# Performance work log

Hardware: AMD Instinct MI355X
Metric: run time of the kernel (lower is better)

## Reference

```python
import jax, jax.numpy as jnp
import numpy as np

L, V, Tctx, D, H, DFF = 4, 32000, 1024, 1024, 16, 4096
HD = D // H
B, T = 2, 1024


def _ln(x, w, b):
    mu = jnp.mean(x, axis=-1, keepdims=True)
    var = jnp.var(x, axis=-1, keepdims=True)
    return (x - mu) * jax.lax.rsqrt(var + 1e-5) * w + b


def setup_inputs() -> dict:
    key = jax.random.key(0)
    ks = jax.random.split(key, 8)
    s = 0.02
    return {
        "idx": jax.random.randint(ks[0], (B, T), 0, V),
        "wte": jax.random.normal(ks[1], (V, D), jnp.float32) * s,
        "wpe": jax.random.normal(ks[2], (Tctx, D), jnp.float32) * s,
        "ln1_w": jnp.ones((L, D), jnp.float32),
        "ln1_b": jnp.zeros((L, D), jnp.float32),
        "qkv_w": jax.random.normal(ks[3], (L, 3 * D, D), jnp.float32) * s,
        "qkv_b": jnp.zeros((L, 3 * D), jnp.float32),
        "proj_w": jax.random.normal(ks[4], (L, D, D), jnp.float32) * s,
        "proj_b": jnp.zeros((L, D), jnp.float32),
        "ln2_w": jnp.ones((L, D), jnp.float32),
        "ln2_b": jnp.zeros((L, D), jnp.float32),
        "fc1_w": jax.random.normal(ks[5], (L, DFF, D), jnp.float32) * s,
        "fc1_b": jnp.zeros((L, DFF), jnp.float32),
        "fc2_w": jax.random.normal(ks[6], (L, D, DFF), jnp.float32) * s,
        "fc2_b": jnp.zeros((L, D), jnp.float32),
        "lnf_w": jnp.ones((D,), jnp.float32),
        "lnf_b": jnp.zeros((D,), jnp.float32),
    }


def reference(idx, wte, wpe, ln1_w, ln1_b, qkv_w, qkv_b, proj_w, proj_b,
              ln2_w, ln2_b, fc1_w, fc1_b, fc2_w, fc2_b, lnf_w, lnf_b):
    b, t = idx.shape
    x = wte[idx] + wpe[:t]  # (B,T,D); dropout=0 (eval)
    scale = 1.0 / jnp.sqrt(jnp.float32(HD))
    causal = jnp.tril(jnp.ones((t, t), bool))  # (T,T)

    def block(x, p):
        (l1w, l1b, qw, qb, pw, pb, l2w, l2b, f1w, f1b, f2w, f2b) = p
        h = _ln(x, l1w, l1b)
        qkv = h @ qw.T + qb  # (B,T,3D)
        q, k, v = jnp.split(qkv, 3, axis=-1)
        q = q.reshape(b, t, H, HD)
        k = k.reshape(b, t, H, HD)
        v = v.reshape(b, t, H, HD)
        att = jnp.einsum('bqhd,bkhd->bhqk', q, k) * scale
        att = jnp.where(causal, att, -jnp.inf)
        att = jax.nn.softmax(att, axis=-1)
        y = jnp.einsum('bhqk,bkhd->bqhd', att, v).reshape(b, t, D)
        x = x + y @ pw.T + pb
        h2 = _ln(x, l2w, l2b)
        h2 = jax.nn.gelu(h2 @ f1w.T + f1b, approximate=False)
        x = x + h2 @ f2w.T + f2b
        return x, None

    params = (ln1_w, ln1_b, qkv_w, qkv_b, proj_w, proj_b,
              ln2_w, ln2_b, fc1_w, fc1_b, fc2_w, fc2_b)
    x, _ = jax.lax.scan(block, x, params)
    x = _ln(x, lnf_w, lnf_b)
    logits = x @ wte.T  # weight-tied lm_head
    return logits
```

## Files before the change

### kernel.cpp

```cpp
#include <hip/hip_runtime.h>
#include <hip/hip_bf16.h>
#include <cstdint>
#include <cstddef>

using hb = __hip_bfloat16;
typedef __bf16 bf16x8 __attribute__((ext_vector_type(8)));
typedef float f32x4 __attribute__((ext_vector_type(4)));
typedef const __attribute__((address_space(1))) void* gptr_t;
typedef __attribute__((address_space(3))) void* lptr_t;

namespace {
constexpr int L_ = 4, V_ = 32000, D_ = 1024, H_ = 16, DFF_ = 4096, HD_ = 64;
constexpr int B_ = 2, T_ = 1024;
constexpr int BT = B_ * T_;
constexpr int PSTR = 56;
constexpr int MTILES = BT / 128;
}

__device__ __forceinline__ void cast_range(const float* __restrict__ in,
                                           hb* __restrict__ out, int n4,
                                           int base, int stride) {
  for (int i = base; i < n4; i += stride) {
    float4 v = reinterpret_cast<const float4*>(in)[i];
    union { hb h[4]; ushort4 u; } t;
    t.h[0] = __float2bfloat16(v.x);
    t.h[1] = __float2bfloat16(v.y);
    t.h[2] = __float2bfloat16(v.z);
    t.h[3] = __float2bfloat16(v.w);
    reinterpret_cast<ushort4*>(out)[i] = t.u;
  }
}

__global__ __launch_bounds__(256) void k_cast5(
    const float* s0, hb* d0, int n0, const float* s1, hb* d1, int n1,
    const float* s2, hb* d2, int n2, const float* s3, hb* d3, int n3,
    const float* s4, hb* d4, int n4) {
  const int base = blockIdx.x * 256 + threadIdx.x;
  const int stride = gridDim.x * 256;
  cast_range(s0, d0, n0, base, stride);
  cast_range(s1, d1, n1, base, stride);
  cast_range(s2, d2, n2, base, stride);
  cast_range(s3, d3, n3, base, stride);
  cast_range(s4, d4, n4, base, stride);
}

__global__ __launch_bounds__(256) void k_embed_ln(const int* __restrict__ idx,
                                                  const float* __restrict__ wte,
                                                  const float* __restrict__ wpe,
                                                  const float* __restrict__ w,
                                                  const float* __restrict__ b,
                                                  float* __restrict__ x,
                                                  hb* __restrict__ out) {
  const int row = blockIdx.x;
  const int tid = threadIdx.x;
  const int t = row & (T_ - 1);
  const int tok = idx[row];
  const float4 a = reinterpret_cast<const float4*>(wte + (size_t)tok * D_)[tid];
  const float4 p = reinterpret_cast<const float4*>(wpe + (size_t)t * D_)[tid];
  const float4 v = {a.x + p.x, a.y + p.y, a.z + p.z, a.w + p.w};
  reinterpret_cast<float4*>(x + (size_t)row * D_)[tid] = v;
  float s = v.x + v.y + v.z + v.w;
  float ss = v.x * v.x + v.y * v.y + v.z * v.z + v.w * v.w;
#pragma unroll
  for (int o = 32; o; o >>= 1) { s += __shfl_xor(s, o); ss += __shfl_xor(ss, o); }
  __shared__ float rs[4], rss[4];
  const int wid = tid >> 6;
  if ((tid & 63) == 0) { rs[wid] = s; rss[wid] = ss; }
  __syncthreads();
  s = rs[0] + rs[1] + rs[2] + rs[3];
  ss = rss[0] + rss[1] + rss[2] + rss[3];
  const float mu = s * (1.f / D_);
  const float var = ss * (1.f / D_) - mu * mu;
  const float rstd = rsqrtf(var + 1e-5f);
  const float4 wv = reinterpret_cast<const float4*>(w)[tid];
  const float4 bv = reinterpret_cast<const float4*>(b)[tid];
  union { hb h[4]; ushort4 u; } o2;
  o2.h[0] = __float2bfloat16((v.x - mu) * rstd * wv.x + bv.x);
  o2.h[1] = __float2bfloat16((v.y - mu) * rstd * wv.y + bv.y);
  o2.h[2] = __float2bfloat16((v.z - mu) * rstd * wv.z + bv.z);
  o2.h[3] = __float2bfloat16((v.w - mu) * rstd * wv.w + bv.w);
  reinterpret_cast<ushort4*>(out + (size_t)row * D_)[tid] = o2.u;
}

__global__ __launch_bounds__(256) void k_ln(const float* __restrict__ x,
                                            const float* __restrict__ w,
                                            const float* __restrict__ b,
                                            hb* __restrict__ out) {
  const int row = blockIdx.x;
  const int tid = threadIdx.x;
  const float4 v = reinterpret_cast<const float4*>(x + (size_t)row * D_)[tid];
  float s = v.x + v.y + v.z + v.w;
  float ss = v.x * v.x + v.y * v.y + v.z * v.z + v.w * v.w;
#pragma unroll
  for (int o = 32; o; o >>= 1) { s += __shfl_xor(s, o); ss += __shfl_xor(ss, o); }
  __shared__ float rs[4], rss[4];
  const int wid = tid >> 6;
  if ((tid & 63) == 0) { rs[wid] = s; rss[wid] = ss; }
  __syncthreads();
  s = rs[0] + rs[1] + rs[2] + rs[3];
  ss = rss[0] + rss[1] + rss[2] + rss[3];
  const float mu = s * (1.f / D_);
  const float var = ss * (1.f / D_) - mu * mu;
  const float rstd = rsqrtf(var + 1e-5f);
  const float4 wv = reinterpret_cast<const float4*>(w)[tid];
  const float4 bv = reinterpret_cast<const float4*>(b)[tid];
  union { hb h[4]; ushort4 u; } t;
  t.h[0] = __float2bfloat16((v.x - mu) * rstd * wv.x + bv.x);
  t.h[1] = __float2bfloat16((v.y - mu) * rstd * wv.y + bv.y);
  t.h[2] = __float2bfloat16((v.z - mu) * rstd * wv.z + bv.z);
  t.h[3] = __float2bfloat16((v.w - mu) * rstd * wv.w + bv.w);
  reinterpret_cast<ushort4*>(out + (size_t)row * D_)[tid] = t.u;
}

__global__ __launch_bounds__(256) void k_attn(const hb* __restrict__ qkv,
                                              const hb* __restrict__ vt,
                                              hb* __restrict__ y) {
  const int lane = threadIdx.x & 63;
  const int wid = threadIdx.x >> 6;
  const int gw = blockIdx.x * 4 + wid;
  const int qt = 63 - (gw & 63);
  const int bh = gw >> 6;
  const int h = bh & (H_ - 1), b = bh >> 4;
  const int q0 = qt * 16;
  const int lr = lane & 15, g = lane >> 4;

  __shared__ __align__(16) hb plds[4][16 * PSTR];
  hb* pw = plds[wid];

  const size_t qrow = ((size_t)(b * T_ + q0 + lr) * 3 * D_) + (size_t)h * HD_;
  const bf16x8 qa0 = *reinterpret_cast<const bf16x8*>(qkv + qrow + g * 8);
  const bf16x8 qa1 = *reinterpret_cast<const bf16x8*>(qkv + qrow + 32 + g * 8);

  const f32x4 z = {0.f, 0.f, 0.f, 0.f};
  float m[4] = {-1e30f, -1e30f, -1e30f, -1e30f};
  float lsum[4] = {0.f, 0.f, 0.f, 0.f};
  f32x4 o[4];
#pragma unroll
  for (int i = 0; i < 4; ++i) o[i] = z;

  const int nkv = (q0 + 47) >> 5;
  for (int kt = 0; kt < nkv; ++kt) {
    const int kv0 = kt * 32;
    f32x4 s[2];
#pragma unroll
    for (int nt = 0; nt < 2; ++nt) {
      const size_t krow =
          ((size_t)(b * T_ + kv0 + nt * 16 + lr) * 3 * D_) + D_ + (size_t)h * HD_;
      const bf16x8 kb0 = *reinterpret_cast<const bf16x8*>(qkv + krow + g * 8);
      const bf16x8 kb1 = *reinterpret_cast<const bf16x8*>(qkv + krow + 32 + g * 8);
      f32x4 acc = z;
      acc = __builtin_amdgcn_mfma_f32_16x16x32_bf16(qa0, kb0, acc, 0, 0, 0);
      acc = __builtin_amdgcn_mfma_f32_16x16x32_bf16(qa1, kb1, acc, 0, 0, 0);
      s[nt] = acc;
    }
#pragma unroll
    for (int r = 0; r < 4; ++r) {
      const int qg = q0 + g * 4 + r;
      const float s0 = (kv0 + lr <= qg) ? s[0][r] * 0.125f : -1e30f;
      const float s1 = (kv0 + 16 + lr <= qg) ? s[1][r] * 0.125f : -1e30f;
      float rmax = fmaxf(s0, s1);
#pragma unroll
      for (int off = 1; off < 16; off <<= 1) rmax = fmaxf(rmax, __shfl_xor(rmax, off));
      const float mn = fmaxf(m[r], rmax);
      const float c = __expf(m[r] - mn);
      m[r] = mn;
      const float p0 = __expf(s0 - mn);
      const float p1 = __expf(s1 - mn);
      float ps = p0 + p1;
#pragma unroll
      for (int off = 1; off < 16; off <<= 1) ps += __shfl_xor(ps, off);
      lsum[r] = lsum[r] * c + ps;
#pragma unroll
      for (int dt = 0; dt < 4; ++dt) o[dt][r] *= c;
      pw[(g * 4 + r) * PSTR + lr] = __float2bfloat16(p0);
      pw[(g * 4 + r) * PSTR + 16 + lr] = __float2bfloat16(p1);
    }
    const bf16x8 pa = *reinterpret_cast<const bf16x8*>(&pw[lr * PSTR + g * 8]);
#pragma unroll
    for (int dt = 0; dt < 4; ++dt) {
      const bf16x8 vb = *reinterpret_cast<const bf16x8*>(
          vt + ((size_t)bh * HD_ + dt * 16 + lr) * T_ + kv0 + g * 8);
      o[dt] = __builtin_amdgcn_mfma_f32_16x16x32_bf16(pa, vb, o[dt], 0, 0, 0);
    }
  }
#pragma unroll
  for (int dt = 0; dt < 4; ++dt) {
#pragma unroll
    for (int r = 0; r < 4; ++r) {
      const size_t oo =
          ((size_t)(b * T_ + q0 + g * 4 + r) * D_) + h * HD_ + dt * 16 + lr;
      y[oo] = __float2bfloat16(o[dt][r] / lsum[r]);
    }
  }
}

template <int EPI, bool OBF, int BN, bool WVT>
__global__ __launch_bounds__(256) void gemm_bt(const hb* __restrict__ A,
                                               const hb* __restrict__ Bw,
                                               const float* __restrict__ bias,
                                               const float* resid,
                                               void* outv, hb* __restrict__ vt,
                                               int M, int N, int K) {
  constexpr int WMR = (BN == 128) ? 4 : 2;
  __shared__ __align__(16) hb As[2][128 * 32];
  __shared__ __align__(16) hb Bs[2][BN * 32];
  const int tid = threadIdx.x, lane = tid & 63, wid = tid >> 6;

  const int nwg = gridDim.x;
  const int d = blockIdx.x;
  const int wg = (d & 7) * (nwg >> 3) + (d >> 3);
  const int m0 = (wg & (MTILES - 1)) * 128;
  const int n0 = (wg / MTILES) * BN;

  const int wr = (BN == 128) ? (wid >> 1) : wid;
  const int wc = (BN == 128) ? (wid & 1) : 0;

  f32x4 acc[WMR][4];
  const f32x4 z = {0.f, 0.f, 0.f, 0.f};
#pragma unroll
  for (int i = 0; i < WMR; ++i)
#pragma unroll
    for (int j = 0; j < 4; ++j) acc[i][j] = z;

  const int e0 = tid * 8;
  auto stage = [&](int buf, int k0) {
#pragma unroll
    for (int r = 0; r < 2; ++r) {
      const int e = e0 + r * 2048;
      const int row = e >> 5, col = e & 31;
      __builtin_amdgcn_global_load_lds(
          (gptr_t)(A + (size_t)(m0 + row) * K + k0 + col), (lptr_t)(&As[buf][e]), 16, 0, 0);
    }
#pragma unroll
    for (int r = 0; r < BN / 64; ++r) {
      const int e = e0 + r * 2048;
      const int row = e >> 5, col = e & 31;
      __builtin_amdgcn_global_load_lds(
          (gptr_t)(Bw + (size_t)(n0 + row) * K + k0 + col), (lptr_t)(&Bs[buf][e]), 16, 0, 0);
    }
  };

  stage(0, 0);
  stage(1, 32);

  const int nt = K >> 5;
  const int lr = lane & 15, lk = (lane >> 4) * 8;
  for (int t = 0; t < nt; ++t) {
    const int cur = t & 1;
    if (t + 1 < nt) {
      if constexpr (BN == 128)
        asm volatile("s_waitcnt vmcnt(4)" ::: "memory");
      else
        asm volatile("s_waitcnt vmcnt(3)" ::: "memory");
    } else {
      asm volatile("s_waitcnt vmcnt(0)" ::: "memory");
    }
    asm volatile("s_barrier" ::: "memory");

    bf16x8 af[WMR], bfr[4];
#pragma unroll
    for (int i = 0; i < WMR; ++i)
      af[i] = *reinterpret_cast<const bf16x8*>(
          &As[cur][(wr * (WMR * 16) + i * 16 + lr) * 32 + lk]);
#pragma unroll
    for (int j = 0; j < 4; ++j)
      bfr[j] = *reinterpret_cast<const bf16x8*>(
          &Bs[cur][(wc * 64 + j * 16 + lr) * 32 + lk]);
#pragma unroll
    for (int i = 0; i < WMR; ++i)
#pragma unroll
      for (int j = 0; j < 4; ++j)
        acc[i][j] = __builtin_amdgcn_mfma_f32_16x16x32_bf16(af[i], bfr[j], acc[i][j], 0, 0, 0);

    asm volatile("s_waitcnt lgkmcnt(0)" ::: "memory");
    asm volatile("s_barrier" ::: "memory");
    if (t + 2 < nt) stage(cur, (t + 2) * 32);
  }

  const int lc = lane & 15, lr4 = (lane >> 4) * 4;
#pragma unroll
  for (int i = 0; i < WMR; ++i) {
    const int grow0 = m0 + wr * (WMR * 16) + i * 16 + lr4;
#pragma unroll
    for (int j = 0; j < 4; ++j) {
      const int gcol = n0 + wc * 64 + j * 16 + lc;
      const float bv = bias ? bias[gcol] : 0.f;
      union { hb h[4]; ushort4 u; } vv;
#pragma unroll
      for (int r = 0; r < 4; ++r) {
        const size_t oo = (size_t)(grow0 + r) * N + gcol;
        float val = acc[i][j][r] + bv;
        if constexpr (EPI == 1) val += resid[oo];
        if constexpr (EPI == 2) val = 0.5f * val * (1.f + erff(val * 0.70710678118f));
        if constexpr (OBF) {
          const hb hv = __float2bfloat16(val);
          reinterpret_cast<hb*>(outv)[oo] = hv;
          if constexpr (WVT) vv.h[r] = hv;
        } else {
          reinterpret_cast<float*>(outv)[oo] = val;
        }
      }
      if constexpr (WVT) {
        if (gcol >= 2 * D_) {
          const int vcol = gcol - 2 * D_;
          const int b = grow0 >> 10;
          const int t0 = grow0 & (T_ - 1);
          *reinterpret_cast<ushort4*>(
              vt + ((size_t)(b * H_ + (vcol >> 6)) * HD_ + (vcol & 63)) * T_ + t0) =
              vv.u;
        }
      }
    }
  }
}

#define MM16(ABASE, AF, BF)                                                     \
  _Pragma("unroll") for (int i_ = 0; i_ < 4; ++i_)                              \
      _Pragma("unroll") for (int j_ = 0; j_ < 4; ++j_)                          \
          acc[(ABASE) + i_][j_] = __builtin_amdgcn_mfma_f32_16x16x32_bf16(      \
              (AF)[i_], (BF)[j_], acc[(ABASE) + i_][j_], 0, 0, 0);

__global__ __launch_bounds__(512, 2) void gemm_lmhead(const hb* __restrict__ A,
                                                      const hb* __restrict__ Bw,
                                                      float* __restrict__ out) {
  constexpr int K = 1024, N = 32000, NT = K / 32;
  __shared__ __align__(16) hb As[4][256][32];
  __shared__ __align__(16) hb Bs[4][256][32];
  const int tid = threadIdx.x, lane = tid & 63, wid = tid >> 6;
  const int nwg = gridDim.x;
  const int dd = blockIdx.x;
  const int wg = (dd & 7) * (nwg >> 3) + (dd >> 3);
  const int m0 = (wg & 7) * 256;
  const int n0 = (wg >> 3) * 256;
  const int wr = wid >> 2, wc = wid & 3;
  const int lr = lane & 15;
  const int rc8 = (((lane >> 4) ^ ((lr >> 1) & 3)) & 3) * 8;

  f32x4 acc[8][4];
  const f32x4 z = {0.f, 0.f, 0.f, 0.f};
#pragma unroll
  for (int i = 0; i < 8; ++i)
#pragma unroll
    for (int j = 0; j < 4; ++j) acc[i][j] = z;

  const int rr = tid >> 2;
  const int cs = tid & 3;
  const int cc = cs ^ ((tid >> 3) & 3);

  auto stageA = [&](int b, int t) {
#pragma unroll
    for (int q = 0; q < 2; ++q) {
      const int row = q * 128 + rr;
      __builtin_amdgcn_global_load_lds(
          (gptr_t)(A + (size_t)(m0 + row) * K + t * 32 + cc * 8),
          (lptr_t)(&As[b][row][cs * 8]), 16, 0, 0);
    }
  };
  auto stageB = [&](int b, int t) {
#pragma unroll
    for (int q = 0; q < 2; ++q) {
      const int row = q * 128 + rr;
      __builtin_amdgcn_global_load_lds(
          (gptr_t)(Bw + (size_t)(n0 + row) * K + t * 32 + cc * 8),
          (lptr_t)(&Bs[b][row][cs * 8]), 16, 0, 0);
    }
  };
  auto dsA = [&](int b, int mh, bf16x8* af) {
#pragma unroll
    for (int i = 0; i < 4; ++i)
      af[i] = *reinterpret_cast<const bf16x8*>(
          &As[b][wr * 128 + mh * 64 + i * 16 + lr][rc8]);
  };
  auto dsB = [&](int b, bf16x8* bf) {
#pragma unroll
    for (int j = 0; j < 4; ++j)
      bf[j] = *reinterpret_cast<const bf16x8*>(&Bs[b][wc * 64 + j * 16 + lr][rc8]);
  };

  auto tile = [&](int t, bool stg, int vm) {
    const int c = t & 3;
    const int b3 = (t + 3) & 3;
    bf16x8 af[4], bf[4];
    dsA(c, 0, af);
    dsB(c, bf);
    if (stg) stageA(b3, t + 3);
    __builtin_amdgcn_s_barrier();
    asm volatile("s_waitcnt lgkmcnt(0)" ::: "memory");
    __builtin_amdgcn_s_setprio(1);
    MM16(0, af, bf)
    __builtin_amdgcn_s_setprio(0);
    __builtin_amdgcn_s_barrier();
    dsA(c, 1, af);
    if (stg) stageB(b3, t + 3);
    if (vm == 8)
      asm volatile("s_waitcnt vmcnt(8)" ::: "memory");
    else if (vm == 4)
      asm volatile("s_waitcnt vmcnt(4)" ::: "memory");
    else if (vm == 0)
      asm volatile("s_waitcnt vmcnt(0)" ::: "memory");
    __builtin_amdgcn_s_barrier();
    asm volatile("s_waitcnt lgkmcnt(0)" ::: "memory");
    __builtin_amdgcn_s_setprio(1);
    MM16(4, af, bf)
    __builtin_amdgcn_s_setprio(0);
    __builtin_amdgcn_s_barrier();
  };

  stageA(0, 0); stageB(0, 0);
  stageA(1, 1); stageB(1, 1);
  stageA(2, 2); stageB(2, 2);
  asm volatile("s_waitcnt vmcnt(8)" ::: "memory");
  __builtin_amdgcn_s_barrier();

  for (int t = 0; t < NT - 3; ++t) tile(t, true, 8);
  tile(NT - 3, false, 4);
  tile(NT - 2, false, 0);
  tile(NT - 1, false, -1);

  const int lc = lane & 15, lr4 = (lane >> 4) * 4;
#pragma unroll
  for (int i2 = 0; i2 < 8; ++i2) {
    const int grow0 = m0 + wr * 128 + i2 * 16 + lr4;
#pragma unroll
    for (int j = 0; j < 4; ++j) {
      const int gcol = n0 + wc * 64 + j * 16 + lc;
#pragma unroll
      for (int r = 0; r < 4; ++r)
        out[(size_t)(grow0 + r) * N + gcol] = acc[i2][j][r];
    }
  }
}

extern "C" void kernel_launch(void* const* d_in, const int* in_sizes, int n_in,
                              void* d_out, int out_size, void* d_ws, size_t ws_size,
                              hipStream_t stream) {
  const int* idx = (const int*)d_in[0];
  const float* wte = (const float*)d_in[1];
  const float* wpe = (const float*)d_in[2];
  const float* ln1_w = (const float*)d_in[3];
  const float* ln1_b = (const float*)d_in[4];
  const float* qkv_w = (const float*)d_in[5];
  const float* qkv_b = (const float*)d_in[6];
  const float* proj_w = (const float*)d_in[7];
  const float* proj_b = (const float*)d_in[8];
  const float* ln2_w = (const float*)d_in[9];
  const float* ln2_b = (const float*)d_in[10];
  const float* fc1_w = (const float*)d_in[11];
  const float* fc1_b = (const float*)d_in[12];
  const float* fc2_w = (const float*)d_in[13];
  const float* fc2_b = (const float*)d_in[14];
  const float* lnf_w = (const float*)d_in[15];
  const float* lnf_b = (const float*)d_in[16];

  char* ws = (char*)d_ws;
  size_t off = 0;
  auto alloc = [&](size_t bytes) -> void* {
    void* p = ws + off;
    off += (bytes + 255) & ~(size_t)255;
    return p;
  };
  hb* wte_bf = (hb*)alloc((size_t)V_ * D_ * 2);
  hb* qkvw_bf = (hb*)alloc((size_t)L_ * 3 * D_ * D_ * 2);
  hb* projw_bf = (hb*)alloc((size_t)L_ * D_ * D_ * 2);
  hb* fc1w_bf = (hb*)alloc((size_t)L_ * DFF_ * D_ * 2);
  hb* fc2w_bf = (hb*)alloc((size_t)L_ * D_ * DFF_ * 2);
  float* x = (float*)alloc((size_t)BT * D_ * 4);
  hb* hbuf = (hb*)alloc((size_t)BT * D_ * 2);
  hb* qkvbuf = (hb*)alloc((size_t)BT * 3 * D_ * 2);
  hb* ybuf = (hb*)alloc((size_t)BT * D_ * 2);
  hb* gbuf = (hb*)alloc((size_t)BT * DFF_ * 2);
  hb* vtbuf = (hb*)alloc((size_t)B_ * H_ * HD_ * T_ * 2);

  k_cast5<<<4096, 256, 0, stream>>>(
      wte, wte_bf, (int)((size_t)V_ * D_ / 4),
      qkv_w, qkvw_bf, (int)((size_t)L_ * 3 * D_ * D_ / 4),
      proj_w, projw_bf, (int)((size_t)L_ * D_ * D_ / 4),
      fc1_w, fc1w_bf, (int)((size_t)L_ * DFF_ * D_ / 4),
      fc2_w, fc2w_bf, (int)((size_t)L_ * D_ * DFF_ / 4));

  k_embed_ln<<<BT, 256, 0, stream>>>(idx, wte, wpe, ln1_w, ln1_b, x, hbuf);

  for (int l = 0; l < L_; ++l) {
    if (l) k_ln<<<BT, 256, 0, stream>>>(x, ln1_w + l * D_, ln1_b + l * D_, hbuf);
    gemm_bt<0, true, 128, true><<<MTILES * (3 * D_ / 128), 256, 0, stream>>>(
        hbuf, qkvw_bf + (size_t)l * 3 * D_ * D_, qkv_b + (size_t)l * 3 * D_, nullptr,
        qkvbuf, vtbuf, BT, 3 * D_, D_);
    k_attn<<<(B_ * H_ * (T_ / 16)) / 4, 256, 0, stream>>>(qkvbuf, vtbuf, ybuf);
    gemm_bt<1, false, 64, false><<<MTILES * (D_ / 64), 256, 0, stream>>>(
        ybuf, projw_bf + (size_t)l * D_ * D_, proj_b + (size_t)l * D_, x, x, nullptr,
        BT, D_, D_);
    k_ln<<<BT, 256, 0, stream>>>(x, ln2_w + l * D_, ln2_b + l * D_, hbuf);
    gemm_bt<2, true, 128, false><<<MTILES * (DFF_ / 128), 256, 0, stream>>>(
        hbuf, fc1w_bf + (size_t)l * DFF_ * D_, fc1_b + (size_t)l * DFF_, nullptr,
        gbuf, nullptr, BT, DFF_, D_);
    gemm_bt<1, false, 64, false><<<MTILES * (D_ / 64), 256, 0, stream>>>(
        gbuf, fc2w_bf + (size_t)l * D_ * DFF_, fc2_b + (size_t)l * D_, x, x, nullptr,
        BT, D_, DFF_);
  }

  k_ln<<<BT, 256, 0, stream>>>(x, lnf_w, lnf_b, hbuf);
  gemm_lmhead<<<8 * (V_ / 256), 512, 0, stream>>>(hbuf, wte_bf, (float*)d_out);
}
```

Before: 1.268 ms.

## Move V transpose to separate kernel and simplify lm_head to double-buffered pipeline

The V transpose is no longer scattered from the QKV GEMM epilogue. It is done by a new LDS-tiled transpose kernel launched before attention, which adds one launch per layer but makes the V^T writes coalesced. Separately, the lm_head GEMM drops its 4-stage LDS ring with split MFMA phases in favour of 2-stage double buffering, halving LDS use and raising the occupancy hint to 4 blocks per CU. The trade is a shallower prefetch depth, with fewer barriers, in exchange for more resident waves.

```diff
diff --git a/kernel.cpp b/kernel.cpp
--- a/kernel.cpp
+++ b/kernel.cpp
@@ -112,6 +112,27 @@
   reinterpret_cast<ushort4*>(out + (size_t)row * D_)[tid] = t.u;
 }
 
+__global__ __launch_bounds__(256) void k_vtrans(const hb* __restrict__ qkv,
+                                                hb* __restrict__ vt) {
+  __shared__ __align__(16) hb tile[64][66];
+  const int bh = blockIdx.x;
+  const int b = bh >> 4, h = bh & (H_ - 1);
+  const int t0 = blockIdx.y * 64;
+  const int tid = threadIdx.x;
+  const int tl = tid >> 2, dc = (tid & 3) * 16;
+  const hb* src = qkv + ((size_t)(b * T_ + t0 + tl) * 3 * D_) + 2 * D_ + h * HD_ + dc;
+  *reinterpret_cast<bf16x8*>(&tile[tl][dc]) = *reinterpret_cast<const bf16x8*>(src);
+  *reinterpret_cast<bf16x8*>(&tile[tl][dc + 8]) = *reinterpret_cast<const bf16x8*>(src + 8);
+  __syncthreads();
+  const int d = tid & 63, tj = tid >> 6;
+  hb o[16];
+#pragma unroll
+  for (int j = 0; j < 16; ++j) o[j] = tile[tj * 16 + j][d];
+  bf16x8* dst = reinterpret_cast<bf16x8*>(vt + ((size_t)bh * HD_ + d) * T_ + t0 + tj * 16);
+  dst[0] = *reinterpret_cast<bf16x8*>(&o[0]);
+  dst[1] = *reinterpret_cast<bf16x8*>(&o[8]);
+}
+
 __global__ __launch_bounds__(256) void k_attn(const hb* __restrict__ qkv,
                                               const hb* __restrict__ vt,
                                               hb* __restrict__ y) {
@@ -194,13 +215,12 @@
   }
 }
 
-template <int EPI, bool OBF, int BN, bool WVT>
+template <int EPI, bool OBF, int BN>
 __global__ __launch_bounds__(256) void gemm_bt(const hb* __restrict__ A,
                                                const hb* __restrict__ Bw,
                                                const float* __restrict__ bias,
                                                const float* resid,
-                                               void* outv, hb* __restrict__ vt,
-                                               int M, int N, int K) {
+                                               void* outv, int M, int N, int K) {
   constexpr int WMR = (BN == 128) ? 4 : 2;
   __shared__ __align__(16) hb As[2][128 * 32];
   __shared__ __align__(16) hb Bs[2][BN * 32];
@@ -285,30 +305,16 @@
     for (int j = 0; j < 4; ++j) {
       const int gcol = n0 + wc * 64 + j * 16 + lc;
       const float bv = bias ? bias[gcol] : 0.f;
-      union { hb h[4]; ushort4 u; } vv;
 #pragma unroll
       for (int r = 0; r < 4; ++r) {
         const size_t oo = (size_t)(grow0 + r) * N + gcol;
         float val = acc[i][j][r] + bv;
         if constexpr (EPI == 1) val += resid[oo];
         if constexpr (EPI == 2) val = 0.5f * val * (1.f + erff(val * 0.70710678118f));
-        if constexpr (OBF) {
-          const hb hv = __float2bfloat16(val);
-          reinterpret_cast<hb*>(outv)[oo] = hv;
-          if constexpr (WVT) vv.h[r] = hv;
-        } else {
+        if constexpr (OBF)
+          reinterpret_cast<hb*>(outv)[oo] = __float2bfloat16(val);
+        else
           reinterpret_cast<float*>(outv)[oo] = val;
-        }
-      }
-      if constexpr (WVT) {
-        if (gcol >= 2 * D_) {
-          const int vcol = gcol - 2 * D_;
-          const int b = grow0 >> 10;
-          const int t0 = grow0 & (T_ - 1);
-          *reinterpret_cast<ushort4*>(
-              vt + ((size_t)(b * H_ + (vcol >> 6)) * HD_ + (vcol & 63)) * T_ + t0) =
-              vv.u;
-        }
       }
     }
   }
@@ -320,12 +326,12 @@
           acc[(ABASE) + i_][j_] = __builtin_amdgcn_mfma_f32_16x16x32_bf16(      \
               (AF)[i_], (BF)[j_], acc[(ABASE) + i_][j_], 0, 0, 0);
 
-__global__ __launch_bounds__(512, 2) void gemm_lmhead(const hb* __restrict__ A,
+__global__ __launch_bounds__(512, 4) void gemm_lmhead(const hb* __restrict__ A,
                                                       const hb* __restrict__ Bw,
                                                       float* __restrict__ out) {
   constexpr int K = 1024, N = 32000, NT = K / 32;
-  __shared__ __align__(16) hb As[4][256][32];
-  __shared__ __align__(16) hb Bs[4][256][32];
+  __shared__ __align__(16) hb As[2][256][32];
+  __shared__ __align__(16) hb Bs[2][256][32];
   const int tid = threadIdx.x, lane = tid & 63, wid = tid >> 6;
   const int nwg = gridDim.x;
   const int dd = blockIdx.x;
@@ -377,45 +383,31 @@
       bf[j] = *reinterpret_cast<const bf16x8*>(&Bs[b][wc * 64 + j * 16 + lr][rc8]);
   };
 
-  auto tile = [&](int t, bool stg, int vm) {
-    const int c = t & 3;
-    const int b3 = (t + 3) & 3;
-    bf16x8 af[4], bf[4];
-    dsA(c, 0, af);
+  auto tile = [&](int t, bool stg, bool last) {
+    const int c = t & 1;
+    if (last)
+      asm volatile("s_waitcnt vmcnt(0)" ::: "memory");
+    else
+      asm volatile("s_waitcnt vmcnt(4)" ::: "memory");
+    __builtin_amdgcn_s_barrier();
+    bf16x8 af0[4], bf[4], af1[4];
+    dsA(c, 0, af0);
     dsB(c, bf);
-    if (stg) stageA(b3, t + 3);
+    dsA(c, 1, af1);
+    __builtin_amdgcn_s_setprio(1);
+    MM16(0, af0, bf)
+    MM16(4, af1, bf)
+    __builtin_amdgcn_s_setprio(0);
+    asm volatile("s_waitcnt lgkmcnt(0)" ::: "memory");
     __builtin_amdgcn_s_barrier();
-    asm volatile("s_waitcnt lgkmcnt(0)" ::: "memory");
-    __builtin_amdgcn_s_setprio(1);
-    MM16(0, af, bf)
-    __builtin_amdgcn_s_setprio(0);
-    __builtin_amdgcn_s_barrier();
-    dsA(c, 1, af);
-    if (stg) stageB(b3, t + 3);
-    if (vm == 8)
-      asm volatile("s_waitcnt vmcnt(8)" ::: "memory");
-    else if (vm == 4)
-      asm volatile("s_waitcnt vmcnt(4)" ::: "memory");
-    else if (vm == 0)
-      asm volatile("s_waitcnt vmcnt(0)" ::: "memory");
-    __builtin_amdgcn_s_barrier();
-    asm volatile("s_waitcnt lgkmcnt(0)" ::: "memory");
-    __builtin_amdgcn_s_setprio(1);
-    MM16(4, af, bf)
-    __builtin_amdgcn_s_setprio(0);
-    __builtin_amdgcn_s_barrier();
+    if (stg) { stageA(c, t + 2); stageB(c, t + 2); }
   };
 
   stageA(0, 0); stageB(0, 0);
   stageA(1, 1); stageB(1, 1);
-  stageA(2, 2); stageB(2, 2);
-  asm volatile("s_waitcnt vmcnt(8)" ::: "memory");
-  __builtin_amdgcn_s_barrier();
-
-  for (int t = 0; t < NT - 3; ++t) tile(t, true, 8);
-  tile(NT - 3, false, 4);
-  tile(NT - 2, false, 0);
-  tile(NT - 1, false, -1);
+
+  for (int t = 0; t < NT - 1; ++t) tile(t, t + 2 < NT, false);
+  tile(NT - 1, false, true);
 
   const int lc = lane & 15, lr4 = (lane >> 4) * 4;
 #pragma unroll
@@ -482,20 +474,19 @@
 
   for (int l = 0; l < L_; ++l) {
     if (l) k_ln<<<BT, 256, 0, stream>>>(x, ln1_w + l * D_, ln1_b + l * D_, hbuf);
-    gemm_bt<0, true, 128, true><<<MTILES * (3 * D_ / 128), 256, 0, stream>>>(
+    gemm_bt<0, true, 128><<<MTILES * (3 * D_ / 128), 256, 0, stream>>>(
         hbuf, qkvw_bf + (size_t)l * 3 * D_ * D_, qkv_b + (size_t)l * 3 * D_, nullptr,
-        qkvbuf, vtbuf, BT, 3 * D_, D_);
+        qkvbuf, BT, 3 * D_, D_);
+    k_vtrans<<<dim3(B_ * H_, T_ / 64), 256, 0, stream>>>(qkvbuf, vtbuf);
     k_attn<<<(B_ * H_ * (T_ / 16)) / 4, 256, 0, stream>>>(qkvbuf, vtbuf, ybuf);
-    gemm_bt<1, false, 64, false><<<MTILES * (D_ / 64), 256, 0, stream>>>(
-        ybuf, projw_bf + (size_t)l * D_ * D_, proj_b + (size_t)l * D_, x, x, nullptr,
-        BT, D_, D_);
+    gemm_bt<1, false, 64><<<MTILES * (D_ / 64), 256, 0, stream>>>(
+        ybuf, projw_bf + (size_t)l * D_ * D_, proj_b + (size_t)l * D_, x, x, BT, D_, D_);
     k_ln<<<BT, 256, 0, stream>>>(x, ln2_w + l * D_, ln2_b + l * D_, hbuf);
-    gemm_bt<2, true, 128, false><<<MTILES * (DFF_ / 128), 256, 0, stream>>>(
+    gemm_bt<2, true, 128><<<MTILES * (DFF_ / 128), 256, 0, stream>>>(
         hbuf, fc1w_bf + (size_t)l * DFF_ * D_, fc1_b + (size_t)l * DFF_, nullptr,
-        gbuf, nullptr, BT, DFF_, D_);
-    gemm_bt<1, false, 64, false><<<MTILES * (D_ / 64), 256, 0, stream>>>(
-        gbuf, fc2w_bf + (size_t)l * D_ * DFF_, fc2_b + (size_t)l * D_, x, x, nullptr,
-        BT, D_, DFF_);
+        gbuf, BT, DFF_, D_);
+    gemm_bt<1, false, 64><<<MTILES * (D_ / 64), 256, 0, stream>>>(
+        gbuf, fc2w_bf + (size_t)l * D_ * DFF_, fc2_b + (size_t)l * D_, x, x, BT, D_, DFF_);
   }
 
   k_ln<<<BT, 256, 0, stream>>>(x, lnf_w, lnf_b, hbuf);
```

After: 2.365 ms. 86.6% more time.
